# Kernel optimization log

Hardware: AMD Instinct MI355X
Metric: run time of the kernel (lower is better)

The kernel has to match this reference:

```python
import jax, jax.numpy as jnp
import numpy as np

D_MODEL = 1024
D_EXPERT = 1024
NUM_EXPERTS = 8
TOP_K = 2


def setup_inputs() -> dict:
    key = jax.random.key(0)
    k_x, k_r, k1, k2, k3 = jax.random.split(key, 5)
    scale = 0.02
    x = jax.random.normal(k_x, (4, 2048, D_MODEL), dtype=jnp.float32)
    Wr = jax.random.normal(k_r, (D_MODEL, NUM_EXPERTS), dtype=jnp.float32) * scale
    # stacked per-expert SwiGLU weights (Linear with bias=False)
    W1 = jax.random.normal(k1, (NUM_EXPERTS, D_MODEL, D_EXPERT), dtype=jnp.float32) * scale
    W2 = jax.random.normal(k2, (NUM_EXPERTS, D_EXPERT, D_MODEL), dtype=jnp.float32) * scale
    W3 = jax.random.normal(k3, (NUM_EXPERTS, D_MODEL, D_EXPERT), dtype=jnp.float32) * scale
    return {"x": x, "Wr": Wr, "W1": W1, "W2": W2, "W3": W3}


def reference(x, Wr, W1, W2, W3):
    B, T, C = x.shape
    xf = x.reshape(-1, C)                       # [N, C], N = B*T
    logits = xf @ Wr                            # [N, E]
    probs = jax.nn.softmax(logits, axis=-1)
    topk_p, topk_i = jax.lax.top_k(probs, TOP_K)  # [N, K]
    topk_p = topk_p / jnp.sum(topk_p, axis=-1, keepdims=True)
    out = jnp.zeros_like(xf)
    for e in range(NUM_EXPERTS):
        # combine weight per token for this expert (0 if not routed here)
        w_e = jnp.sum(topk_p * (topk_i == e), axis=-1)  # [N]
        h = jax.nn.silu(xf @ W1[e]) * (xf @ W3[e])       # [N, d_expert]
        y = h @ W2[e]                                    # [N, C]
        out = out + w_e[:, None] * y
    return out.reshape(B, T, C)
```

## Files before the change

### kernel.cpp

```cpp
#include <hip/hip_runtime.h>
#include <hip/hip_bf16.h>

typedef __attribute__((ext_vector_type(8))) short short8;
typedef __attribute__((ext_vector_type(4))) short short4v;
typedef __attribute__((ext_vector_type(4))) unsigned short ushort4v;
typedef __attribute__((ext_vector_type(4))) float f32x4;

#define NTOK 8192
#define DM 1024
#define DE 1024
#define NE 8

__device__ __forceinline__ float bf2f(unsigned short u) {
  union { unsigned int i; float f; } v; v.i = ((unsigned int)u) << 16; return v.f;
}
__device__ __forceinline__ unsigned short f2bf(float f) {
  union { float f; unsigned int i; } v; v.f = f;
  unsigned int lsb = (v.i >> 16) & 1;
  v.i += 0x7fffu + lsb;
  return (unsigned short)(v.i >> 16);
}
__device__ __forceinline__ void gl_lds(const short* g, short* l) {
  __builtin_amdgcn_global_load_lds((const __attribute__((address_space(1))) void*)g,
                                   (__attribute__((address_space(3))) void*)l, 16, 0, 0);
}

__global__ __launch_bounds__(256) void k_transw(const float* __restrict__ W1,
                                                const float* __restrict__ W2,
                                                const float* __restrict__ W3,
                                                short* __restrict__ wcat,
                                                short* __restrict__ w2t) {
  __shared__ float t[64][65];
  int mid = blockIdx.z;
  const float* src;
  if (mid < 8)       src = W1 + (size_t)mid * (DM * DE);
  else if (mid < 16) src = W3 + (size_t)(mid - 8) * (DM * DE);
  else               src = W2 + (size_t)(mid - 16) * (DE * DM);
  int tid = threadIdx.x;
  int tr = tid >> 4, tc = tid & 15;
  int kbase = blockIdx.y * 64, nbase = blockIdx.x * 64;
#pragma unroll
  for (int j = 0; j < 4; j++) {
    int kr = tr + j * 16;
    f32x4 v = *(const f32x4*)(src + (size_t)(kbase + kr) * 1024 + nbase + tc * 4);
    t[kr][tc * 4 + 0] = v[0]; t[kr][tc * 4 + 1] = v[1];
    t[kr][tc * 4 + 2] = v[2]; t[kr][tc * 4 + 3] = v[3];
  }
  __syncthreads();
#pragma unroll
  for (int j = 0; j < 4; j++) {
    int n = tr + j * 16;
    int ng = nbase + n;
    short4v o;
    o[0] = (short)f2bf(t[tc * 4 + 0][n]);
    o[1] = (short)f2bf(t[tc * 4 + 1][n]);
    o[2] = (short)f2bf(t[tc * 4 + 2][n]);
    o[3] = (short)f2bf(t[tc * 4 + 3][n]);
    size_t dsto;
    if (mid < 16) {
      int e = mid & 7, p = mid >> 3;
      int row_out = ((ng >> 6) * 128) + p * 64 + (ng & 63);
      dsto = (size_t)e * (2048 * 1024) + (size_t)row_out * 1024 + kbase + tc * 4;
      *(short4v*)(wcat + dsto) = o;
    } else {
      int e = mid - 16;
      dsto = (size_t)e * (1024 * 1024) + (size_t)ng * 1024 + kbase + tc * 4;
      *(short4v*)(w2t + dsto) = o;
    }
  }
}

__global__ __launch_bounds__(256) void k_router(const float* __restrict__ x,
                                                const float* __restrict__ Wr,
                                                short* __restrict__ xb,
                                                int* __restrict__ esel,
                                                float* __restrict__ wgt) {
  int wid = threadIdx.x >> 6, lane = threadIdx.x & 63;
  int t = blockIdx.x * 4 + wid;
  const float* xr = x + (size_t)t * DM;
  float acc[8];
#pragma unroll
  for (int e = 0; e < 8; e++) acc[e] = 0.f;
#pragma unroll
  for (int i = 0; i < 4; i++) {
    int kb = (i * 64 + lane) * 4;
    f32x4 v = *(const f32x4*)(xr + kb);
    ushort4v ob;
#pragma unroll
    for (int j = 0; j < 4; j++) {
      f32x4 w0 = *(const f32x4*)(Wr + (size_t)(kb + j) * 8);
      f32x4 w1 = *(const f32x4*)(Wr + (size_t)(kb + j) * 8 + 4);
      float xv = v[j];
      ob[j] = f2bf(xv);
      acc[0] += xv * w0[0]; acc[1] += xv * w0[1];
      acc[2] += xv * w0[2]; acc[3] += xv * w0[3];
      acc[4] += xv * w1[0]; acc[5] += xv * w1[1];
      acc[6] += xv * w1[2]; acc[7] += xv * w1[3];
    }
    *(ushort4v*)(xb + (size_t)t * DM + kb) = ob;
  }
#pragma unroll
  for (int off = 32; off; off >>= 1)
#pragma unroll
    for (int e = 0; e < 8; e++) acc[e] += __shfl_xor(acc[e], off);
  float m0 = -1e30f, m1 = -1e30f; int e0 = 0, e1 = 0;
#pragma unroll
  for (int e = 0; e < 8; e++) {
    float v = acc[e];
    if (v > m0) { m1 = m0; e1 = e0; m0 = v; e0 = e; }
    else if (v > m1) { m1 = v; e1 = e; }
  }
  float p = __expf(m1 - m0);
  if (lane == 0) {
    esel[2 * t] = e0; esel[2 * t + 1] = e1;
    wgt[2 * t] = 1.f / (1.f + p); wgt[2 * t + 1] = p / (1.f + p);
  }
}

__global__ __launch_bounds__(256) void k_rank(const int* __restrict__ esel,
                                              int* __restrict__ cnt,
                                              int* __restrict__ rank) {
  __shared__ int wcnt[4][8];
  __shared__ int woff[4][8];
  int tid = threadIdx.x;
  int lane = tid & 63, wid = tid >> 6;
  int t = blockIdx.x * 256 + tid;
  int e0 = esel[2 * t], e1 = esel[2 * t + 1];
  unsigned long long lt = (lane == 0) ? 0ull : ((~0ull) >> (64 - lane));
  int r0 = 0, r1 = 0;
#pragma unroll
  for (int e = 0; e < 8; e++) {
    unsigned long long m0 = __ballot(e0 == e);
    unsigned long long m1 = __ballot(e1 == e);
    int c0 = __popcll(m0);
    if (e0 == e) r0 = __popcll(m0 & lt);
    if (e1 == e) r1 = c0 + __popcll(m1 & lt);
    if (lane == 0) wcnt[wid][e] = c0 + __popcll(m1);
  }
  __syncthreads();
  if (tid < 8) {
    int e = tid;
    int c0 = wcnt[0][e], c1 = wcnt[1][e], c2 = wcnt[2][e], c3 = wcnt[3][e];
    int base = atomicAdd(&cnt[e], c0 + c1 + c2 + c3);
    woff[0][e] = base;
    woff[1][e] = base + c0;
    woff[2][e] = base + c0 + c1;
    woff[3][e] = base + c0 + c1 + c2;
  }
  __syncthreads();
  rank[2 * t] = woff[wid][e0] + r0;
  rank[2 * t + 1] = woff[wid][e1] + r1;
}

__global__ void k_offsets(const int* __restrict__ cnt, int* __restrict__ off) {
  if (threadIdx.x == 0) {
    int s = 0;
    for (int e = 0; e < NE; e++) { off[e] = s; s += cnt[e]; }
  }
}

__global__ __launch_bounds__(256) void k_scatter(const int* __restrict__ off,
                                                 const int* __restrict__ esel,
                                                 const int* __restrict__ rank,
                                                 int* __restrict__ tok_of_slot,
                                                 int* __restrict__ slot_of_tok) {
  int t = blockIdx.x * 256 + threadIdx.x;
#pragma unroll
  for (int j = 0; j < 2; j++) {
    int e = esel[2 * t + j];
    int s = off[e] + rank[2 * t + j];
    tok_of_slot[s] = t;
    slot_of_tok[2 * t + j] = s;
  }
}

template<int FFN1>
__global__ __launch_bounds__(256, 2) void k_ffn(const short* __restrict__ Abase,
                                                const short* __restrict__ Bbase,
                                                const int* __restrict__ cnt,
                                                const int* __restrict__ off,
                                                const int* __restrict__ tok_of_slot,
                                                short* __restrict__ outp) {
  const int e = blockIdx.y;
  const int cnt_e = cnt[e];
  const int m0 = blockIdx.z * 256;
  if (m0 >= cnt_e) return;
  const int bse = off[e];
  const int nt = blockIdx.x;
  const short* Bt = Bbase + (size_t)e * ((FFN1 ? 2048 : 1024) * 1024) + (size_t)(nt * 128) * 1024;

  __shared__ __align__(128) short Al[3][8192];
  __shared__ __align__(128) short Bl[3][4096];

  const int tid = threadIdx.x;
  const int lane = tid & 63, wid = tid >> 6;
  const int wr = wid >> 1, wcn = wid & 1;

  const short* srcA[4]; const short* srcB[2];
#pragma unroll
  for (int i = 0; i < 4; i++) {
    int ch = tid + i * 256;
    int r = ch >> 2, c = (ch & 3) ^ ((r >> 1) & 3);
    int row = m0 + r; if (row >= cnt_e) row = cnt_e - 1;
    long ar = FFN1 ? (long)tok_of_slot[bse + row] : (long)(bse + row);
    srcA[i] = Abase + ar * 1024 + c * 8;
    if (i < 2) srcB[i] = Bt + (size_t)r * 1024 + c * 8;
  }

  int aoff[8], boff[4];
#pragma unroll
  for (int m = 0; m < 8; m++) {
    int r = wr * 128 + m * 16 + (lane & 15);
    aoff[m] = (r * 4 + ((lane >> 4) ^ ((r >> 1) & 3))) * 16;
  }
#pragma unroll
  for (int n = 0; n < 4; n++) {
    int rb = FFN1 ? (wcn * 32 + (n & 1) * 16 + (n >> 1) * 64 + (lane & 15))
                  : (wcn * 64 + n * 16 + (lane & 15));
    boff[n] = (rb * 4 + ((lane >> 4) ^ ((rb >> 1) & 3))) * 16;
  }

  f32x4 acc[8][4];
#pragma unroll
  for (int m = 0; m < 8; m++)
#pragma unroll
    for (int n = 0; n < 4; n++) acc[m][n] = (f32x4){0.f, 0.f, 0.f, 0.f};

#define STG_A(b, kt) { gl_lds(srcA[0] + (kt) * 32, &Al[b][(tid + 0) * 8]); \
                       gl_lds(srcA[1] + (kt) * 32, &Al[b][(tid + 256) * 8]); \
                       gl_lds(srcA[2] + (kt) * 32, &Al[b][(tid + 512) * 8]); \
                       gl_lds(srcA[3] + (kt) * 32, &Al[b][(tid + 768) * 8]); }
#define STG_B(b, kt) { gl_lds(srcB[0] + (kt) * 32, &Bl[b][(tid + 0) * 8]); \
                       gl_lds(srcB[1] + (kt) * 32, &Bl[b][(tid + 256) * 8]); }

  STG_A(0, 0); STG_B(0, 0);
  STG_A(1, 1); STG_B(1, 1);
  asm volatile("s_waitcnt vmcnt(6)" ::: "memory");
  __builtin_amdgcn_s_barrier();

  int cur = 0, nxt = 2;
  for (int t = 0; t < 32; ++t) {
    int ktn = (t + 2 < 32) ? (t + 2) : 31;
    const char* Ab = (const char*)Al[cur];
    const char* Bb = (const char*)Bl[cur];
    short8 a[8], b[4];
#pragma unroll
    for (int m = 0; m < 8; m++) a[m] = *(const short8*)(Ab + aoff[m]);
#pragma unroll
    for (int n = 0; n < 4; n++) b[n] = *(const short8*)(Bb + boff[n]);
    STG_A(nxt, ktn); STG_B(nxt, ktn);
    __builtin_amdgcn_s_setprio(1);
#pragma unroll
    for (int m = 0; m < 8; m++)
#pragma unroll
      for (int n = 0; n < 4; n++)
        acc[m][n] = __builtin_amdgcn_mfma_f32_16x16x32_bf16(a[m], b[n], acc[m][n], 0, 0, 0);
    __builtin_amdgcn_s_setprio(0);
    asm volatile("s_waitcnt vmcnt(6)" ::: "memory");
    __builtin_amdgcn_s_barrier();
    cur = (cur == 2) ? 0 : cur + 1;
    nxt = (nxt == 2) ? 0 : nxt + 1;
  }
  asm volatile("s_waitcnt vmcnt(0)" ::: "memory");

  if (FFN1) {
#pragma unroll
    for (int m = 0; m < 8; m++)
#pragma unroll
      for (int cc = 0; cc < 2; cc++) {
        f32x4 v1 = acc[m][cc], v3 = acc[m][cc + 2];
        int col = nt * 64 + wcn * 32 + cc * 16 + (lane & 15);
#pragma unroll
        for (int i = 0; i < 4; i++) {
          int row = m0 + wr * 128 + m * 16 + ((lane >> 4) * 4) + i;
          if (row < cnt_e) {
            float a1v = v1[i];
            float hv = (a1v / (1.f + __expf(-a1v))) * v3[i];
            outp[(size_t)(bse + row) * DE + col] = (short)f2bf(hv);
          }
        }
      }
  } else {
#pragma unroll
    for (int m = 0; m < 8; m++)
#pragma unroll
      for (int n = 0; n < 4; n++) {
        f32x4 v = acc[m][n];
        int col = nt * 128 + wcn * 64 + n * 16 + (lane & 15);
#pragma unroll
        for (int i = 0; i < 4; i++) {
          int row = m0 + wr * 128 + m * 16 + ((lane >> 4) * 4) + i;
          if (row < cnt_e)
            outp[(size_t)(bse + row) * DM + col] = (short)f2bf(v[i]);
        }
      }
  }
}

__global__ __launch_bounds__(256) void k_combine(const short* __restrict__ y,
                                                 const int* __restrict__ slot_of_tok,
                                                 const float* __restrict__ wgt,
                                                 float* __restrict__ out) {
  int t = blockIdx.x;
  int s0 = slot_of_tok[2 * t], s1 = slot_of_tok[2 * t + 1];
  float w0 = wgt[2 * t], w1 = wgt[2 * t + 1];
  int c = threadIdx.x * 4;
  short4v a = *(const short4v*)(y + (size_t)s0 * DM + c);
  short4v b = *(const short4v*)(y + (size_t)s1 * DM + c);
  f32x4 o;
#pragma unroll
  for (int j = 0; j < 4; j++)
    o[j] = w0 * bf2f((unsigned short)a[j]) + w1 * bf2f((unsigned short)b[j]);
  *(f32x4*)(out + (size_t)t * DM + c) = o;
}

extern "C" void kernel_launch(void* const* d_in, const int* in_sizes, int n_in,
                              void* d_out, int out_size, void* d_ws, size_t ws_size,
                              hipStream_t stream) {
  const float* x  = (const float*)d_in[0];
  const float* Wr = (const float*)d_in[1];
  const float* W1 = (const float*)d_in[2];
  const float* W2 = (const float*)d_in[3];
  const float* W3 = (const float*)d_in[4];
  float* out = (float*)d_out;
  char* ws = (char*)d_ws;

  short* xb   = (short*)(ws);
  short* wcat = (short*)(ws + 16777216);
  short* w2t  = (short*)(ws + 50331648);
  short* h    = (short*)(ws + 67108864);
  short* y    = (short*)(ws + 100663296);
  char* meta = ws + 134217728;
  int* cnt          = (int*)(meta);
  int* off          = (int*)(meta + 256);
  int* esel         = (int*)(meta + 512);
  int* rank         = (int*)(meta + 512 + 65536);
  int* tok_of_slot  = (int*)(meta + 512 + 2 * 65536);
  int* slot_of_tok  = (int*)(meta + 512 + 3 * 65536);
  float* wgt        = (float*)(meta + 512 + 4 * 65536);

  hipMemsetAsync(cnt, 0, 32, stream);
  k_transw<<<dim3(16, 16, 24), 256, 0, stream>>>(W1, W2, W3, wcat, w2t);
  k_router<<<2048, 256, 0, stream>>>(x, Wr, xb, esel, wgt);
  k_rank<<<32, 256, 0, stream>>>(esel, cnt, rank);
  k_offsets<<<1, 64, 0, stream>>>(cnt, off);
  k_scatter<<<32, 256, 0, stream>>>(off, esel, rank, tok_of_slot, slot_of_tok);
  k_ffn<1><<<dim3(16, 8, 32), 256, 0, stream>>>(xb, wcat, cnt, off, tok_of_slot, h);
  k_ffn<0><<<dim3(8, 8, 32), 256, 0, stream>>>(h, w2t, cnt, off, tok_of_slot, y);
  k_combine<<<8192, 256, 0, stream>>>(y, slot_of_tok, wgt, out);
}
```

Baseline: 250.2 us.

## Shrink expert GEMM M-tile to 128 and switch to double-buffered register prefetch

The grouped FFN GEMM kernels drop from 256-row to 128-row tiles, doubling the number of M blocks and raising the launch-bounds occupancy hint from 2 to 3. Shared-memory staging goes from a triple-buffered A/B ring to two buffers. LDS fragments for the next k-step are now prefetched into registers while the MFMAs for the current step run. The aim is more resident blocks and better latency hiding on smaller register and LDS footprints. The cost is lower arithmetic intensity per tile and a full vmcnt(0) drain every k-step, which limits how far global loads can run ahead.

```diff
diff --git a/kernel.cpp b/kernel.cpp
--- a/kernel.cpp
+++ b/kernel.cpp
@@ -175,7 +175,7 @@
 }
 
 template<int FFN1>
-__global__ __launch_bounds__(256, 2) void k_ffn(const short* __restrict__ Abase,
+__global__ __launch_bounds__(256, 3) void k_ffn(const short* __restrict__ Abase,
                                                 const short* __restrict__ Bbase,
                                                 const int* __restrict__ cnt,
                                                 const int* __restrict__ off,
@@ -183,34 +183,34 @@
                                                 short* __restrict__ outp) {
   const int e = blockIdx.y;
   const int cnt_e = cnt[e];
-  const int m0 = blockIdx.z * 256;
+  const int m0 = blockIdx.z * 128;
   if (m0 >= cnt_e) return;
   const int bse = off[e];
   const int nt = blockIdx.x;
   const short* Bt = Bbase + (size_t)e * ((FFN1 ? 2048 : 1024) * 1024) + (size_t)(nt * 128) * 1024;
 
-  __shared__ __align__(128) short Al[3][8192];
-  __shared__ __align__(128) short Bl[3][4096];
+  __shared__ __align__(128) short Al[2][4096];
+  __shared__ __align__(128) short Bl[2][4096];
 
   const int tid = threadIdx.x;
   const int lane = tid & 63, wid = tid >> 6;
   const int wr = wid >> 1, wcn = wid & 1;
 
-  const short* srcA[4]; const short* srcB[2];
-#pragma unroll
-  for (int i = 0; i < 4; i++) {
+  const short* srcA[2]; const short* srcB[2];
+#pragma unroll
+  for (int i = 0; i < 2; i++) {
     int ch = tid + i * 256;
     int r = ch >> 2, c = (ch & 3) ^ ((r >> 1) & 3);
     int row = m0 + r; if (row >= cnt_e) row = cnt_e - 1;
     long ar = FFN1 ? (long)tok_of_slot[bse + row] : (long)(bse + row);
     srcA[i] = Abase + ar * 1024 + c * 8;
-    if (i < 2) srcB[i] = Bt + (size_t)r * 1024 + c * 8;
-  }
-
-  int aoff[8], boff[4];
-#pragma unroll
-  for (int m = 0; m < 8; m++) {
-    int r = wr * 128 + m * 16 + (lane & 15);
+    srcB[i] = Bt + (size_t)r * 1024 + c * 8;
+  }
+
+  int aoff[4], boff[4];
+#pragma unroll
+  for (int m = 0; m < 4; m++) {
+    int r = wr * 64 + m * 16 + (lane & 15);
     aoff[m] = (r * 4 + ((lane >> 4) ^ ((r >> 1) & 3))) * 16;
   }
 #pragma unroll
@@ -220,59 +220,66 @@
     boff[n] = (rb * 4 + ((lane >> 4) ^ ((rb >> 1) & 3))) * 16;
   }
 
-  f32x4 acc[8][4];
-#pragma unroll
-  for (int m = 0; m < 8; m++)
+  f32x4 acc[4][4];
+#pragma unroll
+  for (int m = 0; m < 4; m++)
 #pragma unroll
     for (int n = 0; n < 4; n++) acc[m][n] = (f32x4){0.f, 0.f, 0.f, 0.f};
 
-#define STG_A(b, kt) { gl_lds(srcA[0] + (kt) * 32, &Al[b][(tid + 0) * 8]); \
-                       gl_lds(srcA[1] + (kt) * 32, &Al[b][(tid + 256) * 8]); \
-                       gl_lds(srcA[2] + (kt) * 32, &Al[b][(tid + 512) * 8]); \
-                       gl_lds(srcA[3] + (kt) * 32, &Al[b][(tid + 768) * 8]); }
-#define STG_B(b, kt) { gl_lds(srcB[0] + (kt) * 32, &Bl[b][(tid + 0) * 8]); \
-                       gl_lds(srcB[1] + (kt) * 32, &Bl[b][(tid + 256) * 8]); }
-
-  STG_A(0, 0); STG_B(0, 0);
-  STG_A(1, 1); STG_B(1, 1);
-  asm volatile("s_waitcnt vmcnt(6)" ::: "memory");
+#define STG(P, kt) { gl_lds(srcA[0] + (kt) * 32, &Al[P][(tid + 0) * 8]); \
+                     gl_lds(srcA[1] + (kt) * 32, &Al[P][(tid + 256) * 8]); \
+                     gl_lds(srcB[0] + (kt) * 32, &Bl[P][(tid + 0) * 8]); \
+                     gl_lds(srcB[1] + (kt) * 32, &Bl[P][(tid + 256) * 8]); }
+
+  short8 a0[4], b0[4], a1[4], b1[4];
+
+  STG(0, 0); STG(1, 1);
+  asm volatile("s_waitcnt vmcnt(4)" ::: "memory");
   __builtin_amdgcn_s_barrier();
-
-  int cur = 0, nxt = 2;
-  for (int t = 0; t < 32; ++t) {
-    int ktn = (t + 2 < 32) ? (t + 2) : 31;
-    const char* Ab = (const char*)Al[cur];
-    const char* Bb = (const char*)Bl[cur];
-    short8 a[8], b[4];
-#pragma unroll
-    for (int m = 0; m < 8; m++) a[m] = *(const short8*)(Ab + aoff[m]);
-#pragma unroll
-    for (int n = 0; n < 4; n++) b[n] = *(const short8*)(Bb + boff[n]);
-    STG_A(nxt, ktn); STG_B(nxt, ktn);
-    __builtin_amdgcn_s_setprio(1);
-#pragma unroll
-    for (int m = 0; m < 8; m++)
-#pragma unroll
-      for (int n = 0; n < 4; n++)
-        acc[m][n] = __builtin_amdgcn_mfma_f32_16x16x32_bf16(a[m], b[n], acc[m][n], 0, 0, 0);
-    __builtin_amdgcn_s_setprio(0);
-    asm volatile("s_waitcnt vmcnt(6)" ::: "memory");
-    __builtin_amdgcn_s_barrier();
-    cur = (cur == 2) ? 0 : cur + 1;
-    nxt = (nxt == 2) ? 0 : nxt + 1;
-  }
+  {
+    const char* An = (const char*)Al[0];
+    const char* Bn = (const char*)Bl[0];
+#pragma unroll
+    for (int m = 0; m < 4; m++) a0[m] = *(const short8*)(An + aoff[m]);
+#pragma unroll
+    for (int n = 0; n < 4; n++) b0[n] = *(const short8*)(Bn + boff[n]);
+  }
+  asm volatile("s_waitcnt lgkmcnt(0)" ::: "memory");
   asm volatile("s_waitcnt vmcnt(0)" ::: "memory");
+  __builtin_amdgcn_s_barrier();
+
+#define STEP(T, P, CA, CB, NA, NB) { \
+    const int ktn = ((T) + 2 < 32) ? (T) + 2 : 31; \
+    STG(P, ktn); \
+    const char* An = (const char*)Al[(P) ^ 1]; \
+    const char* Bn = (const char*)Bl[(P) ^ 1]; \
+    _Pragma("unroll") for (int m = 0; m < 4; m++) NA[m] = *(const short8*)(An + aoff[m]); \
+    _Pragma("unroll") for (int n = 0; n < 4; n++) NB[n] = *(const short8*)(Bn + boff[n]); \
+    __builtin_amdgcn_s_setprio(1); \
+    _Pragma("unroll") for (int m = 0; m < 4; m++) \
+      _Pragma("unroll") for (int n = 0; n < 4; n++) \
+        acc[m][n] = __builtin_amdgcn_mfma_f32_16x16x32_bf16(CA[m], CB[n], acc[m][n], 0, 0, 0); \
+    __builtin_amdgcn_s_setprio(0); \
+    asm volatile("s_waitcnt lgkmcnt(0)" ::: "memory"); \
+    asm volatile("s_waitcnt vmcnt(0)" ::: "memory"); \
+    __builtin_amdgcn_s_barrier(); }
+
+  for (int t2 = 0; t2 < 16; ++t2) {
+    const int t = t2 * 2;
+    STEP(t,     0, a0, b0, a1, b1);
+    STEP(t + 1, 1, a1, b1, a0, b0);
+  }
 
   if (FFN1) {
 #pragma unroll
-    for (int m = 0; m < 8; m++)
+    for (int m = 0; m < 4; m++)
 #pragma unroll
       for (int cc = 0; cc < 2; cc++) {
         f32x4 v1 = acc[m][cc], v3 = acc[m][cc + 2];
         int col = nt * 64 + wcn * 32 + cc * 16 + (lane & 15);
 #pragma unroll
         for (int i = 0; i < 4; i++) {
-          int row = m0 + wr * 128 + m * 16 + ((lane >> 4) * 4) + i;
+          int row = m0 + wr * 64 + m * 16 + ((lane >> 4) * 4) + i;
           if (row < cnt_e) {
             float a1v = v1[i];
             float hv = (a1v / (1.f + __expf(-a1v))) * v3[i];
@@ -282,14 +289,14 @@
       }
   } else {
 #pragma unroll
-    for (int m = 0; m < 8; m++)
+    for (int m = 0; m < 4; m++)
 #pragma unroll
       for (int n = 0; n < 4; n++) {
         f32x4 v = acc[m][n];
         int col = nt * 128 + wcn * 64 + n * 16 + (lane & 15);
 #pragma unroll
         for (int i = 0; i < 4; i++) {
-          int row = m0 + wr * 128 + m * 16 + ((lane >> 4) * 4) + i;
+          int row = m0 + wr * 64 + m * 16 + ((lane >> 4) * 4) + i;
           if (row < cnt_e)
             outp[(size_t)(bse + row) * DM + col] = (short)f2bf(v[i]);
         }
@@ -345,7 +352,7 @@
   k_rank<<<32, 256, 0, stream>>>(esel, cnt, rank);
   k_offsets<<<1, 64, 0, stream>>>(cnt, off);
   k_scatter<<<32, 256, 0, stream>>>(off, esel, rank, tok_of_slot, slot_of_tok);
-  k_ffn<1><<<dim3(16, 8, 32), 256, 0, stream>>>(xb, wcat, cnt, off, tok_of_slot, h);
-  k_ffn<0><<<dim3(8, 8, 32), 256, 0, stream>>>(h, w2t, cnt, off, tok_of_slot, y);
+  k_ffn<1><<<dim3(16, 8, 64), 256, 0, stream>>>(xb, wcat, cnt, off, tok_of_slot, h);
+  k_ffn<0><<<dim3(8, 8, 64), 256, 0, stream>>>(h, w2t, cnt, off, tok_of_slot, y);
   k_combine<<<8192, 256, 0, stream>>>(y, slot_of_tok, wgt, out);
 }
```

Result: no change. 246.2 us (-1.6%).
